# Kernel tuning notes

Hardware: AMD Instinct MI355X
Metric: run time of the kernel (lower is better)

Reference implementation:

```python
import jax, jax.numpy as jnp
import numpy as np

D_MODEL = 1024
N_TILES = 16
N_CLASSES = 1024
BATCH = 65536
THRESH = 0.3  # ternary quantization threshold


def setup_inputs() -> dict:
    key = jax.random.key(0)
    k_x, k_s, k_w, k_b = jax.random.split(key, 4)
    x = jax.random.normal(k_x, (BATCH, D_MODEL), dtype=jnp.float32)
    # signatures_raw: n_tiles params of shape [d_model], init randn*0.5
    sigs_raw = jax.random.normal(k_s, (N_TILES, D_MODEL), dtype=jnp.float32) * 0.5
    # per-tile Linear(d_model, n_classes): weight [n_classes, d_model], bias [n_classes]
    lim = 1.0 / np.sqrt(D_MODEL)
    W = jax.random.uniform(k_w, (N_TILES, N_CLASSES, D_MODEL), dtype=jnp.float32, minval=-lim, maxval=lim)
    b = jax.random.uniform(k_b, (N_TILES, N_CLASSES), dtype=jnp.float32, minval=-lim, maxval=lim)
    return {"x": x, "sigs_raw": sigs_raw, "W": W, "b": b}


def _quantize_ternary(s):
    # straight-through ternary: forward = {-1, 0, +1}, backward = identity
    q = jnp.where(s > THRESH, 1.0, jnp.where(s < -THRESH, -1.0, 0.0)).astype(s.dtype)
    return s + jax.lax.stop_gradient(q - s)


def reference(x, sigs_raw, W, b):
    sigs = _quantize_ternary(sigs_raw)           # [T, D]
    scores = x @ sigs.T                          # [B, T]
    tile_indices = jnp.argmax(scores, axis=-1)   # [B]
    n_tiles = W.shape[0]
    logits = jnp.zeros((x.shape[0], W.shape[1]), dtype=x.dtype)  # [B, C]
    # fixed small loop over tiles (experts); select per-token result via mask
    for t in range(n_tiles):
        out_t = x @ W[t].T + b[t]                # [B, C]
        logits = jnp.where((tile_indices == t)[:, None], out_t, logits)
    return logits, tile_indices
```

## Files before the change

kernel.cpp:

```cpp
#include <hip/hip_runtime.h>
#include <hip/hip_bf16.h>
#include <stdint.h>

#define B_TOK 65536
#define DM 1024
#define NC 1024
#define NT 16
#define GAPTHR 0.25f

typedef __attribute__((ext_vector_type(4))) float f32x4;
typedef __attribute__((ext_vector_type(4))) unsigned int u32x4;
typedef __attribute__((ext_vector_type(2))) unsigned int u32x2;
typedef __attribute__((ext_vector_type(4))) unsigned short u16x4;
typedef __attribute__((ext_vector_type(8))) short short8;

#define AS1(p) ((__attribute__((address_space(1))) void*)(p))
#define AS3(p) ((__attribute__((address_space(3))) void*)(p))

static __device__ inline unsigned short f2bf(float f) {
  __hip_bfloat16 h = __float2bfloat16(f);
  unsigned short u;
  __builtin_memcpy(&u, &h, 2);
  return u;
}
#define PK8(a, b, old, w) __builtin_amdgcn_cvt_pk_fp8_f32((a), (b), (old), (w))

__global__ void k_prep(const float* __restrict__ sigs, unsigned int* __restrict__ mask,
                       unsigned short* __restrict__ Sb, int* __restrict__ ctrl) {
  int d = threadIdx.x;
  if (d < 64) ctrl[d] = 0;
  unsigned int m = 0;
#pragma unroll
  for (int t = 0; t < NT; ++t) {
    float s = sigs[t * DM + d];
    float q = (s > 0.3f) ? 1.0f : ((s < -0.3f) ? -1.0f : 0.0f);
    if (s > 0.3f) m |= 1u << t;
    else if (s < -0.3f) m |= 1u << (16 + t);
    Sb[t * DM + d] = f2bf(q);
  }
  mask[d] = m;
}

__global__ __launch_bounds__(256) void k_pre(const float* __restrict__ x,
    const unsigned short* __restrict__ Sb, unsigned char* __restrict__ xb,
    int* __restrict__ tidx, float* __restrict__ oidx,
    int* __restrict__ fixlist, int* __restrict__ nfix, int* __restrict__ counts,
    const float* __restrict__ W, unsigned char* __restrict__ Wb)
{
  int bid = blockIdx.x;
  int tid = threadIdx.x;
  if (bid >= 1024) {
    const f32x4* W4 = (const f32x4*)W;
    unsigned int* O = (unsigned int*)Wb;
    int n4 = NT * NC * DM / 4;
    for (int i = (bid - 1024) * 256 + tid; i < n4; i += 512 * 256) {
      f32x4 v = W4[i];
      unsigned int p = PK8(v[0] * 16.f, v[1] * 16.f, 0, 0);
      p = PK8(v[2] * 16.f, v[3] * 16.f, p, 1);
      O[i] = p;
    }
    return;
  }
  __shared__ int hist[16];
  if (tid < 16) hist[tid] = 0;
  __syncthreads();

  int w = tid >> 6, l = tid & 63;
  int lr = l & 15, lg = l >> 4;
  int tok0 = bid * 64 + w * 16;

  const float* xr = x + (size_t)(tok0 + lr) * DM + lg * 8;
  unsigned char* xbr = xb + (size_t)(tok0 + lr) * DM + lg * 8;
  const unsigned short* sr = Sb + (size_t)lr * DM + lg * 8;

  f32x4 accA = (f32x4){0.f, 0.f, 0.f, 0.f};
  f32x4 accB = (f32x4){0.f, 0.f, 0.f, 0.f};
  for (int kc = 0; kc < 32; kc += 2) {
    f32x4 v0 = *(const f32x4*)(xr + kc * 32);
    f32x4 v1 = *(const f32x4*)(xr + kc * 32 + 4);
    f32x4 v2 = *(const f32x4*)(xr + kc * 32 + 32);
    f32x4 v3 = *(const f32x4*)(xr + kc * 32 + 36);
    short8 a0, a1;
#pragma unroll
    for (int j = 0; j < 4; ++j) {
      a0[j]     = (short)f2bf(v0[j]);
      a0[4 + j] = (short)f2bf(v1[j]);
      a1[j]     = (short)f2bf(v2[j]);
      a1[4 + j] = (short)f2bf(v3[j]);
    }
    u32x2 p0, p1;
    p0[0] = PK8(v0[0], v0[1], 0, 0); p0[0] = PK8(v0[2], v0[3], p0[0], 1);
    p0[1] = PK8(v1[0], v1[1], 0, 0); p0[1] = PK8(v1[2], v1[3], p0[1], 1);
    p1[0] = PK8(v2[0], v2[1], 0, 0); p1[0] = PK8(v2[2], v2[3], p1[0], 1);
    p1[1] = PK8(v3[0], v3[1], 0, 0); p1[1] = PK8(v3[2], v3[3], p1[1], 1);
    *(u32x2*)(xbr + kc * 32) = p0;
    *(u32x2*)(xbr + kc * 32 + 32) = p1;
    short8 b0 = *(const short8*)(sr + kc * 32);
    short8 b1 = *(const short8*)(sr + kc * 32 + 32);
    accA = __builtin_amdgcn_mfma_f32_16x16x32_bf16(a0, b0, accA, 0, 0, 0);
    accB = __builtin_amdgcn_mfma_f32_16x16x32_bf16(a1, b1, accB, 0, 0, 0);
  }
  f32x4 acc;
#pragma unroll
  for (int i = 0; i < 4; ++i) acc[i] = accA[i] + accB[i];

  float m1[4], m2v[4]; int i1[4];
#pragma unroll
  for (int i = 0; i < 4; ++i) { m1[i] = acc[i]; i1[i] = lr; m2v[i] = -1e30f; }
#pragma unroll
  for (int off = 1; off < 16; off <<= 1) {
#pragma unroll
    for (int i = 0; i < 4; ++i) {
      float bm  = __shfl_xor(m1[i], off);
      int   bi  = __shfl_xor(i1[i], off);
      float bm2 = __shfl_xor(m2v[i], off);
      bool bwin = (bm > m1[i]) || (bm == m1[i] && bi < i1[i]);
      float loser = bwin ? m1[i] : bm;
      m2v[i] = fmaxf(fmaxf(m2v[i], bm2), loser);
      if (bwin) { m1[i] = bm; i1[i] = bi; }
    }
  }
  if (lr == 0) {
#pragma unroll
    for (int i = 0; i < 4; ++i) {
      int tok = tok0 + lg * 4 + i;
      tidx[tok] = i1[i];
      oidx[tok] = (float)i1[i];
      atomicAdd(&hist[i1[i]], 1);
      if (m1[i] - m2v[i] < GAPTHR) {
        int p = atomicAdd(nfix, 1);
        fixlist[p] = tok;
      }
    }
  }
  __syncthreads();
  if (tid < 16 && hist[tid]) atomicAdd(&counts[tid], hist[tid]);
}

__global__ __launch_bounds__(256) void k_fix(const float* __restrict__ x,
    const unsigned int* __restrict__ mask, const int* __restrict__ fixlist,
    const int* __restrict__ nfix, int* __restrict__ tidx, float* __restrict__ oidx,
    int* __restrict__ counts)
{
  int n = *nfix;
  int l = threadIdx.x & 63;
  int gw = (blockIdx.x * 256 + threadIdx.x) >> 6;
  int nw = (gridDim.x * 256) >> 6;
  int t = l & 15, seg = l >> 4;

  for (int i = gw; i < n; i += nw) {
    int tok = fixlist[i];
    const float* xr = x + (size_t)tok * DM + seg * 256;
    const unsigned int* mr = mask + seg * 256;
    double acc0 = 0.0, acc1 = 0.0;
    for (int j = 0; j < 256; j += 4) {
      f32x4 xv = *(const f32x4*)(xr + j);
      u32x4 mv = *(const u32x4*)(mr + j);
#pragma unroll
      for (int u = 0; u < 4; ++u) {
        double c = ((mv[u] >> t) & 1u) ? (double)xv[u]
                 : (((mv[u] >> (16 + t)) & 1u) ? -(double)xv[u] : 0.0);
        if (u & 1) acc1 += c; else acc0 += c;
      }
    }
    double s = acc0 + acc1;
    s += __shfl_xor(s, 16);
    s += __shfl_xor(s, 32);
    double bv = s; int bi = t;
#pragma unroll
    for (int off = 1; off < 16; off <<= 1) {
      double ov = __shfl_xor(bv, off);
      int   oi = __shfl_xor(bi, off);
      if (ov > bv || (ov == bv && oi < bi)) { bv = ov; bi = oi; }
    }
    if (l == 0) {
      int old = tidx[tok];
      if (bi != old) {
        tidx[tok] = bi;
        oidx[tok] = (float)bi;
        atomicSub(&counts[old], 1);
        atomicAdd(&counts[bi], 1);
      }
    }
  }
}

__global__ void k_scan(const int* __restrict__ counts, int* __restrict__ offs,
                       int* __restrict__ perm) {
  __shared__ int so[NT + 1], sc[NT];
  if (threadIdx.x == 0) {
    int s = 0;
    for (int t = 0; t < NT; ++t) {
      so[t] = s; offs[t] = s;
      sc[t] = counts[t];
      s += (counts[t] + 255) & ~255;
    }
    so[NT] = s; offs[NT] = s;
  }
  __syncthreads();
  for (int t = 0; t < NT; ++t) {
    int start = so[t] + sc[t], end = so[t + 1];
    for (int i = start + threadIdx.x; i < end; i += blockDim.x) perm[i] = -1;
  }
}

__global__ __launch_bounds__(256) void k_place(const int* __restrict__ tidx, const int* __restrict__ offs,
                                               int* __restrict__ cursor, int* __restrict__ perm) {
  __shared__ int h[16], base[16];
  int tid = threadIdx.x;
  if (tid < 16) h[tid] = 0;
  __syncthreads();
  int tok = blockIdx.x * 256 + tid;
  int t = tidx[tok];
  int myloc = atomicAdd(&h[t], 1);
  __syncthreads();
  if (tid < 16 && h[tid]) base[tid] = atomicAdd(&cursor[tid], h[tid]);
  __syncthreads();
  perm[offs[t] + base[t] + myloc] = tok;
}

__global__ __launch_bounds__(512, 2) void k_gemm(const unsigned char* __restrict__ xb,
    const unsigned char* __restrict__ Wb, const float* __restrict__ bias,
    const int* __restrict__ perm, const int* __restrict__ offs, float* __restrict__ out)
{
  __shared__ unsigned char lds[4][2][256 * 32];
  int bid0 = blockIdx.x;
  int bid = (bid0 & 7) * 136 + (bid0 >> 3);
  int mb = bid >> 2, nb = bid & 3;
  int total = offs[NT];
  int m0 = mb << 8;
  if (m0 >= total) return;
  int t = 0;
#pragma unroll
  for (int tt = 0; tt < NT; ++tt) if (m0 >= offs[tt + 1]) t = tt + 1;
  int c0 = nb << 8;
  int tid = threadIdx.x;

  int srow = tid >> 1;
  int sk = (((tid & 1) ^ ((tid >> 3) & 1)) << 4);
  int tkA = perm[m0 + srow]; if (tkA < 0) tkA = 0;
  const unsigned char* pA = xb + (size_t)tkA * DM + sk;
  const unsigned char* pB = Wb + (size_t)t * NC * DM + (size_t)(c0 + srow) * DM + sk;

  f32x4 acc[8][4];
#pragma unroll
  for (int m = 0; m < 8; ++m)
#pragma unroll
    for (int n = 0; n < 4; ++n) acc[m][n] = (f32x4){0.f, 0.f, 0.f, 0.f};

  int wid = tid >> 6, l = tid & 63;
  int wr = wid >> 2, wc = wid & 3;
  int lr = l & 15, lk = l >> 4;
  int wr128 = wr * 128, wc64 = wc * 64;
  int goff = (lk ^ (((lr >> 2) & 1) << 1)) * 8;

#define GLDS(g, lp) __builtin_amdgcn_global_load_lds(AS1(g), AS3(lp), 16, 0, 0)
#define STAGE_A(SS, KT) GLDS(pA + (KT) * 32, &lds[SS][0][tid * 16])
#define STAGE_B(SS, KT) GLDS(pB + (KT) * 32, &lds[SS][1][tid * 16])
#define RD_A(SLOT, M) (*(const long*)&lds[SLOT][0][(wr128 + (M) * 16 + lr) * 32 + goff])
#define RD_B(SLOT, N) (*(const long*)&lds[SLOT][1][(wc64 + (N) * 16 + lr) * 32 + goff])
#define MF(M_, N_, AV, BV) acc[M_][N_] = __builtin_amdgcn_mfma_f32_16x16x32_fp8_fp8(AV, BV, acc[M_][N_], 0, 0, 0)
#define MFMA4(M_, AV) { MF(M_, 0, AV, b0); MF(M_, 1, AV, b1); MF(M_, 2, AV, b2); MF(M_, 3, AV, b3); }
#define VM4() asm volatile("s_waitcnt vmcnt(4)" ::: "memory")
#define VM2() asm volatile("s_waitcnt vmcnt(2)" ::: "memory")
#define VM0() asm volatile("s_waitcnt vmcnt(0)" ::: "memory")

#define KTILE(KT, SLOT, SS, DOSTAGE, VMW) { \
  long b0 = RD_B(SLOT, 0), b1 = RD_B(SLOT, 1), b2 = RD_B(SLOT, 2), b3 = RD_B(SLOT, 3); \
  long a0 = RD_A(SLOT, 0), a1 = RD_A(SLOT, 1); \
  if (DOSTAGE) STAGE_A(SS, (KT) + 3); \
  __builtin_amdgcn_s_setprio(1); \
  MFMA4(0, a0); MFMA4(1, a1); \
  { long a2 = RD_A(SLOT, 2), a3 = RD_A(SLOT, 3); \
    if (DOSTAGE) STAGE_B(SS, (KT) + 3); \
    MFMA4(2, a2); MFMA4(3, a3); } \
  { long a4 = RD_A(SLOT, 4), a5 = RD_A(SLOT, 5); MFMA4(4, a4); MFMA4(5, a5); } \
  { long a6 = RD_A(SLOT, 6), a7 = RD_A(SLOT, 7); MFMA4(6, a6); MFMA4(7, a7); } \
  __builtin_amdgcn_s_setprio(0); \
  VMW; \
  __builtin_amdgcn_s_barrier(); }

  STAGE_A(0, 0); STAGE_B(0, 0);
  STAGE_A(1, 1); STAGE_B(1, 1);
  STAGE_A(2, 2); STAGE_B(2, 2);
  VM4();
  __builtin_amdgcn_s_barrier();

#pragma unroll 1
  for (int kt = 0; kt < 28; kt += 4) {
    KTILE(kt + 0, 0, 3, 1, VM4());
    KTILE(kt + 1, 1, 0, 1, VM4());
    KTILE(kt + 2, 2, 1, 1, VM4());
    KTILE(kt + 3, 3, 2, 1, VM4());
  }
  KTILE(28, 0, 3, 1, VM4());
  KTILE(29, 1, 0, 0, VM2());
  KTILE(30, 2, 1, 0, VM0());
  KTILE(31, 3, 2, 0, ((void)0));

  float bv[4];
#pragma unroll
  for (int n = 0; n < 4; ++n) bv[n] = bias[t * NC + c0 + wc64 + n * 16 + lr];
#pragma unroll
  for (int m = 0; m < 8; ++m) {
#pragma unroll
    for (int j = 0; j < 4; ++j) {
      int prow = m0 + wr128 + m * 16 + lk * 4 + j;
      int tok = perm[prow];
      if (tok >= 0) {
#pragma unroll
        for (int n = 0; n < 4; ++n)
          out[(size_t)tok * NC + c0 + wc64 + n * 16 + lr] = acc[m][n][j] * 0.0625f + bv[n];
      }
    }
  }
}

extern "C" void kernel_launch(void* const* d_in, const int* in_sizes, int n_in,
                              void* d_out, int out_size, void* d_ws, size_t ws_size,
                              hipStream_t stream) {
  const float* x    = (const float*)d_in[0];
  const float* sigs = (const float*)d_in[1];
  const float* W    = (const float*)d_in[2];
  const float* bias = (const float*)d_in[3];
  float* out = (float*)d_out;
  float* oidx = out + (size_t)B_TOK * NC;

  char* ws = (char*)d_ws;
  unsigned char* xb    = (unsigned char*)ws;
  unsigned char* Wb    = (unsigned char*)(ws + 67108864);
  int* perm            = (int*)(ws + 83886080);
  int* tidx            = (int*)(ws + 84164608);
  unsigned int* mask   = (unsigned int*)(ws + 84426752);
  unsigned short* Sb   = (unsigned short*)(ws + 84430848);
  int* fixlist         = (int*)(ws + 84463616);
  int* ctrl            = (int*)(ws + 84725760);
  int* counts = ctrl;
  int* cursor = ctrl + 16;
  int* offs   = ctrl + 32;
  int* nfix   = ctrl + 49;

  k_prep<<<1, 1024, 0, stream>>>(sigs, mask, Sb, ctrl);
  k_pre<<<1536, 256, 0, stream>>>(x, Sb, xb, tidx, oidx, fixlist, nfix, counts, W, Wb);
  k_fix<<<512, 256, 0, stream>>>(x, mask, fixlist, nfix, tidx, oidx, counts);
  k_scan<<<1, 256, 0, stream>>>(counts, offs, perm);
  k_place<<<256, 256, 0, stream>>>(tidx, offs, cursor, perm);
  k_gemm<<<dim3(272 * 4), 512, 0, stream>>>(xb, Wb, bias, perm, offs, out);
}
```

Measured before the change: 316.8 us.

## Deepen GEMM LDS pipeline to six stages and fold scan kernel into place/gemm

The separate scan kernel is removed. Segment offsets are now computed inline in k_place and k_gemm from the per-tile counts, and padded rows are bounded by a per-segment limit instead of -1 sentinels in perm. The GEMM main loop moves from a 4-slot, one-tile-per-step LDS ring to a 6-slot ring that processes two K-tiles per barrier, which halves the barrier count. The k_fix grid is also halved. The cost is LDS per block growing to 96KB, which may not let two blocks co-reside per CU as the launch bounds intend, so occupancy could drop.

```diff
diff --git a/kernel.cpp b/kernel.cpp
--- a/kernel.cpp
+++ b/kernel.cpp
@@ -185,29 +185,15 @@
   }
 }
 
-__global__ void k_scan(const int* __restrict__ counts, int* __restrict__ offs,
-                       int* __restrict__ perm) {
-  __shared__ int so[NT + 1], sc[NT];
-  if (threadIdx.x == 0) {
+__global__ __launch_bounds__(256) void k_place(const int* __restrict__ tidx, const int* __restrict__ counts,
+                                               int* __restrict__ cursor, int* __restrict__ perm) {
+  __shared__ int h[16], base[16], offs_s[16];
+  int tid = threadIdx.x;
+  if (tid == 0) {
     int s = 0;
-    for (int t = 0; t < NT; ++t) {
-      so[t] = s; offs[t] = s;
-      sc[t] = counts[t];
-      s += (counts[t] + 255) & ~255;
-    }
-    so[NT] = s; offs[NT] = s;
-  }
-  __syncthreads();
-  for (int t = 0; t < NT; ++t) {
-    int start = so[t] + sc[t], end = so[t + 1];
-    for (int i = start + threadIdx.x; i < end; i += blockDim.x) perm[i] = -1;
-  }
-}
-
-__global__ __launch_bounds__(256) void k_place(const int* __restrict__ tidx, const int* __restrict__ offs,
-                                               int* __restrict__ cursor, int* __restrict__ perm) {
-  __shared__ int h[16], base[16];
-  int tid = threadIdx.x;
+#pragma unroll
+    for (int tt = 0; tt < NT; ++tt) { offs_s[tt] = s; s += (counts[tt] + 255) & ~255; }
+  }
   if (tid < 16) h[tid] = 0;
   __syncthreads();
   int tok = blockIdx.x * 256 + tid;
@@ -216,29 +202,39 @@
   __syncthreads();
   if (tid < 16 && h[tid]) base[tid] = atomicAdd(&cursor[tid], h[tid]);
   __syncthreads();
-  perm[offs[t] + base[t] + myloc] = tok;
+  perm[offs_s[t] + base[t] + myloc] = tok;
 }
 
 __global__ __launch_bounds__(512, 2) void k_gemm(const unsigned char* __restrict__ xb,
     const unsigned char* __restrict__ Wb, const float* __restrict__ bias,
-    const int* __restrict__ perm, const int* __restrict__ offs, float* __restrict__ out)
+    const int* __restrict__ perm, const int* __restrict__ counts, float* __restrict__ out)
 {
-  __shared__ unsigned char lds[4][2][256 * 32];
+  __shared__ unsigned char lds[6][2][256 * 32];
   int bid0 = blockIdx.x;
   int bid = (bid0 & 7) * 136 + (bid0 >> 3);
   int mb = bid >> 2, nb = bid & 3;
-  int total = offs[NT];
   int m0 = mb << 8;
-  if (m0 >= total) return;
-  int t = 0;
-#pragma unroll
-  for (int tt = 0; tt < NT; ++tt) if (m0 >= offs[tt + 1]) t = tt + 1;
+
+  int t = NT, seg_base = 0, cnt = 0;
+  {
+    int s = 0;
+#pragma unroll
+    for (int tt = 0; tt < NT; ++tt) {
+      int c = counts[tt];
+      int pad = (c + 255) & ~255;
+      if (m0 >= s && m0 < s + pad) { t = tt; seg_base = s; cnt = c; }
+      s += pad;
+    }
+    if (m0 >= s || t == NT) return;
+  }
+  int limit = seg_base + cnt;
   int c0 = nb << 8;
   int tid = threadIdx.x;
 
   int srow = tid >> 1;
   int sk = (((tid & 1) ^ ((tid >> 3) & 1)) << 4);
-  int tkA = perm[m0 + srow]; if (tkA < 0) tkA = 0;
+  int pidx = m0 + srow; if (pidx >= limit) pidx = seg_base;
+  int tkA = perm[pidx];
   const unsigned char* pA = xb + (size_t)tkA * DM + sk;
   const unsigned char* pB = Wb + (size_t)t * NC * DM + (size_t)(c0 + srow) * DM + sk;
 
@@ -262,41 +258,45 @@
 #define MF(M_, N_, AV, BV) acc[M_][N_] = __builtin_amdgcn_mfma_f32_16x16x32_fp8_fp8(AV, BV, acc[M_][N_], 0, 0, 0)
 #define MFMA4(M_, AV) { MF(M_, 0, AV, b0); MF(M_, 1, AV, b1); MF(M_, 2, AV, b2); MF(M_, 3, AV, b3); }
 #define VM4() asm volatile("s_waitcnt vmcnt(4)" ::: "memory")
-#define VM2() asm volatile("s_waitcnt vmcnt(2)" ::: "memory")
 #define VM0() asm volatile("s_waitcnt vmcnt(0)" ::: "memory")
 
-#define KTILE(KT, SLOT, SS, DOSTAGE, VMW) { \
+#define HALF(SLOT, SS, KT4, DOSTAGE) { \
   long b0 = RD_B(SLOT, 0), b1 = RD_B(SLOT, 1), b2 = RD_B(SLOT, 2), b3 = RD_B(SLOT, 3); \
   long a0 = RD_A(SLOT, 0), a1 = RD_A(SLOT, 1); \
-  if (DOSTAGE) STAGE_A(SS, (KT) + 3); \
+  if (DOSTAGE) STAGE_A(SS, KT4); \
   __builtin_amdgcn_s_setprio(1); \
   MFMA4(0, a0); MFMA4(1, a1); \
   { long a2 = RD_A(SLOT, 2), a3 = RD_A(SLOT, 3); \
-    if (DOSTAGE) STAGE_B(SS, (KT) + 3); \
+    if (DOSTAGE) STAGE_B(SS, KT4); \
     MFMA4(2, a2); MFMA4(3, a3); } \
   { long a4 = RD_A(SLOT, 4), a5 = RD_A(SLOT, 5); MFMA4(4, a4); MFMA4(5, a5); } \
   { long a6 = RD_A(SLOT, 6), a7 = RD_A(SLOT, 7); MFMA4(6, a6); MFMA4(7, a7); } \
-  __builtin_amdgcn_s_setprio(0); \
+  __builtin_amdgcn_s_setprio(0); }
+
+#define SSTEP(KT, SA, SB, T0, T1, DOSTAGE, VMW) { \
+  HALF(SA, T0, (KT) + 4, DOSTAGE); \
+  HALF(SB, T1, (KT) + 5, DOSTAGE); \
   VMW; \
   __builtin_amdgcn_s_barrier(); }
 
   STAGE_A(0, 0); STAGE_B(0, 0);
   STAGE_A(1, 1); STAGE_B(1, 1);
   STAGE_A(2, 2); STAGE_B(2, 2);
+  STAGE_A(3, 3); STAGE_B(3, 3);
   VM4();
   __builtin_amdgcn_s_barrier();
 
 #pragma unroll 1
-  for (int kt = 0; kt < 28; kt += 4) {
-    KTILE(kt + 0, 0, 3, 1, VM4());
-    KTILE(kt + 1, 1, 0, 1, VM4());
-    KTILE(kt + 2, 2, 1, 1, VM4());
-    KTILE(kt + 3, 3, 2, 1, VM4());
-  }
-  KTILE(28, 0, 3, 1, VM4());
-  KTILE(29, 1, 0, 0, VM2());
-  KTILE(30, 2, 1, 0, VM0());
-  KTILE(31, 3, 2, 0, ((void)0));
+  for (int s3 = 0; s3 < 4; ++s3) {
+    int kt = s3 * 6;
+    SSTEP(kt + 0, 0, 1, 4, 5, 1, VM4());
+    SSTEP(kt + 2, 2, 3, 0, 1, 1, VM4());
+    SSTEP(kt + 4, 4, 5, 2, 3, 1, VM4());
+  }
+  SSTEP(24, 0, 1, 4, 5, 1, VM4());
+  SSTEP(26, 2, 3, 0, 1, 1, VM4());
+  SSTEP(28, 4, 5, 0, 0, 0, VM0());
+  SSTEP(30, 0, 1, 0, 0, 0, ((void)0));
 
   float bv[4];
 #pragma unroll
@@ -306,8 +306,8 @@
 #pragma unroll
     for (int j = 0; j < 4; ++j) {
       int prow = m0 + wr128 + m * 16 + lk * 4 + j;
-      int tok = perm[prow];
-      if (tok >= 0) {
+      if (prow < limit) {
+        int tok = perm[prow];
 #pragma unroll
         for (int n = 0; n < 4; ++n)
           out[(size_t)tok * NC + c0 + wc64 + n * 16 + lr] = acc[m][n][j] * 0.0625f + bv[n];
@@ -337,13 +337,11 @@
   int* ctrl            = (int*)(ws + 84725760);
   int* counts = ctrl;
   int* cursor = ctrl + 16;
-  int* offs   = ctrl + 32;
   int* nfix   = ctrl + 49;
 
   k_prep<<<1, 1024, 0, stream>>>(sigs, mask, Sb, ctrl);
   k_pre<<<1536, 256, 0, stream>>>(x, Sb, xb, tidx, oidx, fixlist, nfix, counts, W, Wb);
-  k_fix<<<512, 256, 0, stream>>>(x, mask, fixlist, nfix, tidx, oidx, counts);
-  k_scan<<<1, 256, 0, stream>>>(counts, offs, perm);
-  k_place<<<256, 256, 0, stream>>>(tidx, offs, cursor, perm);
-  k_gemm<<<dim3(272 * 4), 512, 0, stream>>>(xb, Wb, bias, perm, offs, out);
-}
+  k_fix<<<256, 256, 0, stream>>>(x, mask, fixlist, nfix, tidx, oidx, counts);
+  k_place<<<256, 256, 0, stream>>>(tidx, counts, cursor, perm);
+  k_gemm<<<dim3(272 * 4), 512, 0, stream>>>(xb, Wb, bias, perm, counts, out);
+}
```

Measured after the change: 321.8 us. About the same (+1.6%).
